# Kernel optimization log

Measured on AMD Instinct MI355X. Metric: run time of the kernel, lower is better.

The kernel has to match this reference:

```python
import jax, jax.numpy as jnp
import numpy as np
from jax.scipy.special import logsumexp

T = 8192        # trajectory length
S_DIM = 256     # state feature dim
B_OPT = 64      # number of options b
N_ACT = 64      # number of actions
STOP_IX = 0     # STOP_NET_STOP_IX
CONT_IX = 1     # STOP_NET_CONTINUE_IX


def setup_inputs() -> dict:
    key = jax.random.key(0)
    k1, k2, k3, k4, k5 = jax.random.split(key, 5)
    s_i = jax.random.normal(k1, (T + 1, S_DIM), dtype=jnp.float32)
    W_action = jax.random.normal(k2, (S_DIM, B_OPT, N_ACT), dtype=jnp.float32) * 0.02
    W_stop = jax.random.normal(k3, (S_DIM, B_OPT, 2), dtype=jnp.float32) * 0.02
    W_start = jax.random.normal(k4, (S_DIM, B_OPT), dtype=jnp.float32) * 0.02
    actions = jax.random.randint(k5, (T,), 0, N_ACT, dtype=jnp.int32)
    return {"s_i": s_i, "W_action": W_action, "W_stop": W_stop,
            "W_start": W_start, "actions": actions, "lengths": T}


def reference(s_i, W_action, W_stop, W_start, actions, lengths):
    # control_net heads: per-state, per-option log-probabilities
    action_logps = jax.nn.log_softmax(jnp.einsum('ts,sbn->tbn', s_i, W_action), axis=-1)  # (T+1, b, n_act)
    stop_logps = jax.nn.log_softmax(jnp.einsum('ts,sbc->tbc', s_i, W_stop), axis=-1)      # (T+1, b, 2)
    start_logps = jax.nn.log_softmax(jnp.einsum('ts,sb->tb', s_i, W_start), axis=-1)      # (T+1, b)

    Tn = actions.shape[0]
    # emission logp of the taken action at each step: (T, b)
    emit = jnp.take_along_axis(action_logps[:Tn], actions[:, None, None].astype(jnp.int32), axis=2)[:, :, 0]

    f0 = start_logps[0] + emit[0]  # (b,)
    eye = jnp.eye(B_OPT, dtype=bool)
    neg_inf = jnp.float32(-jnp.inf)

    def step(f_prev, xs):
        beta, one_minus_beta, start, em = xs
        # trans[i, j] = logaddexp(beta_i + start_j, delta_ij * log(1-beta_i))
        cont = jnp.where(eye, one_minus_beta[:, None], neg_inf)
        trans = jnp.logaddexp(beta[:, None] + start[None, :], cont)
        f = logsumexp(f_prev[:, None] + trans + em[None, :], axis=0)
        return f, None

    xs = (stop_logps[1:Tn, :, STOP_IX], stop_logps[1:Tn, :, CONT_IX],
          start_logps[1:Tn], emit[1:])
    f, _ = jax.lax.scan(step, f0, xs)

    total_logp = logsumexp(f + stop_logps[Tn, :, STOP_IX])
    return -total_logp
```

## Files before the change

### kernel.cpp

```cpp
#include <hip/hip_runtime.h>
#include <stdint.h>


typedef short bf16x8 __attribute__((ext_vector_type(8)));
typedef float f32x4  __attribute__((ext_vector_type(4)));
typedef unsigned short u16;

#define T_LEN 8192
#define SDIM  256

#define WS_SBF    0
#define WS_WAT    4227072
#define WS_WSMT   6324224
#define WS_PE     6422528
#define WS_PS     8519680
#define WS_PB     10617088
#define WS_PC     12714496
#define WS_MOUT   14811904
#define WS_LSC    16909056
#define WS_GOUT   WS_PC
#define WS_GLSC   (WS_PC + 262144)

__device__ inline u16 f2bf(float f) {
  union { float f; uint32_t u; } v; v.f = f;
  uint32_t u = v.u;
  return (u16)((u + 0x7fffu + ((u >> 16) & 1u)) >> 16);
}

__global__ void conv_s(const float* __restrict__ s_i, u16* __restrict__ s_bf) {
  int idx = blockIdx.x * 256 + threadIdx.x;
  int t = idx >> 8;
  float v = (t < T_LEN + 1) ? s_i[idx] : 0.f;
  s_bf[idx] = f2bf(v);
}

__global__ void conv_wa(const float* __restrict__ Wa, u16* __restrict__ wa_t) {
  int idx = blockIdx.x * 256 + threadIdx.x;
  int s = idx >> 12, bn = idx & 4095;
  wa_t[bn * 256 + s] = f2bf(Wa[idx]);
}

__global__ void conv_wsm(const float* __restrict__ Wstop, const float* __restrict__ Wstart,
                         u16* __restrict__ wsm_t) {
  int idx = blockIdx.x * 256 + threadIdx.x;
  int col = idx >> 8, s = idx & 255;
  float v;
  if (col < 64)       v = Wstart[s * 64 + col];
  else if (col < 128) v = Wstop[s * 128 + (col - 64) * 2 + 0];
  else                v = Wstop[s * 128 + (col - 128) * 2 + 1];
  wsm_t[col * 256 + s] = f2bf(v);
}

__global__ __launch_bounds__(256, 4) void act_gemm(
    const u16* __restrict__ s_bf, const u16* __restrict__ wa_t,
    const int* __restrict__ actions, float* __restrict__ peT) {
  __shared__ uint4 ldsB[64 * 32];
  const int tid = threadIdx.x;
  const int lane = tid & 63;
  const int wm = tid >> 6;
  const int g = lane >> 4, c = lane & 15;

  int bid = blockIdx.x;
  int swz = (bid & 7) * 512 + (bid >> 3);
  const int t0 = (swz >> 6) * 128;
  const int b0 = swz & 63;

  const int tbase = t0 + wm * 32;

  int act[2][4];
#pragma unroll
  for (int mf = 0; mf < 2; ++mf)
#pragma unroll
    for (int q = 0; q < 4; ++q)
      act[mf][q] = actions[tbase + mf * 16 + g * 4 + q];

  const u16* aRow0 = s_bf + (size_t)(tbase + c) * 256;
  const u16* aRow1 = s_bf + (size_t)(tbase + 16 + c) * 256;

  bf16x8 af0[2][4];
#pragma unroll
  for (int ks = 0; ks < 4; ++ks) {
    af0[0][ks] = *(const bf16x8*)(aRow0 + ks * 32 + g * 8);
    af0[1][ks] = *(const bf16x8*)(aRow1 + ks * 32 + g * 8);
  }

  {
    const u16* bsrc = wa_t + (size_t)b0 * 64 * 256;
#pragma unroll
    for (int it = 0; it < 8; ++it) {
      int i = tid + 256 * it;
      int r = i >> 5, s = i & 31;
      ldsB[r * 32 + (s ^ (r & 7))] = *(const uint4*)(bsrc + r * 256 + s * 8);
    }
  }
  __syncthreads();

  f32x4 acc[2][4];
#pragma unroll
  for (int mf = 0; mf < 2; ++mf)
#pragma unroll
    for (int nf = 0; nf < 4; ++nf) acc[mf][nf] = (f32x4){0.f, 0.f, 0.f, 0.f};

  bf16x8 af1[2][4];
#pragma unroll
  for (int ks = 0; ks < 4; ++ks) {
    af1[0][ks] = *(const bf16x8*)(aRow0 + 128 + ks * 32 + g * 8);
    af1[1][ks] = *(const bf16x8*)(aRow1 + 128 + ks * 32 + g * 8);
  }

#pragma unroll
  for (int ks = 0; ks < 4; ++ks) {
#pragma unroll
    for (int nf = 0; nf < 4; ++nf) {
      int rr = nf * 16 + c;
      bf16x8 bfv = *(const bf16x8*)&ldsB[rr * 32 + ((ks * 4 + g) ^ (rr & 7))];
      acc[0][nf] = __builtin_amdgcn_mfma_f32_16x16x32_bf16(af0[0][ks], bfv, acc[0][nf], 0, 0, 0);
      acc[1][nf] = __builtin_amdgcn_mfma_f32_16x16x32_bf16(af0[1][ks], bfv, acc[1][nf], 0, 0, 0);
    }
  }
#pragma unroll
  for (int ks = 0; ks < 4; ++ks) {
#pragma unroll
    for (int nf = 0; nf < 4; ++nf) {
      int rr = nf * 16 + c;
      bf16x8 bfv = *(const bf16x8*)&ldsB[rr * 32 + (((ks + 4) * 4 + g) ^ (rr & 7))];
      acc[0][nf] = __builtin_amdgcn_mfma_f32_16x16x32_bf16(af1[0][ks], bfv, acc[0][nf], 0, 0, 0);
      acc[1][nf] = __builtin_amdgcn_mfma_f32_16x16x32_bf16(af1[1][ks], bfv, acc[1][nf], 0, 0, 0);
    }
  }

  const size_t pebase = (size_t)b0 * 8192;
#pragma unroll
  for (int mf = 0; mf < 2; ++mf) {
#pragma unroll
    for (int q = 0; q < 4; ++q) {
      float e0 = __expf(acc[mf][0][q]);
      float e1 = __expf(acc[mf][1][q]);
      float e2 = __expf(acc[mf][2][q]);
      float e3 = __expf(acc[mf][3][q]);
      float s = (e0 + e1) + (e2 + e3);
#pragma unroll
      for (int d = 1; d < 16; d <<= 1) s += __shfl_xor(s, d);
      int a = act[mf][q];
      int acf = a >> 4;
      float esel = (acf == 0) ? e0 : (acf == 1) ? e1 : (acf == 2) ? e2 : e3;
      if (c == (a & 15))
        peT[pebase + tbase + mf * 16 + g * 4 + q] = esel / s;
    }
  }
}

__global__ __launch_bounds__(256) void small_gemm(
    const u16* __restrict__ s_bf, const u16* __restrict__ wsm_t,
    float* __restrict__ ps, float* __restrict__ pb, float* __restrict__ pc) {
  __shared__ uint4 ldsA[64 * 16];
  __shared__ uint4 ldsB[192 * 16];
  const int t0 = blockIdx.x * 64;
  const int tid = threadIdx.x;
  const int lane = tid & 63, w = tid >> 6;
  const int g = lane >> 4, c = lane & 15;

  f32x4 acc[12];
#pragma unroll
  for (int i = 0; i < 12; ++i) acc[i] = (f32x4){0.f, 0.f, 0.f, 0.f};

  for (int kh = 0; kh < 2; ++kh) {
    if (kh) __syncthreads();
    for (int i = tid; i < 64 * 16; i += 256) {
      int row = i >> 4, u = i & 15;
      ldsA[(row * 16 + u) ^ (row & 7)] =
          *(const uint4*)(s_bf + (size_t)(t0 + row) * 256 + kh * 128 + u * 8);
    }
    for (int i = tid; i < 192 * 16; i += 256) {
      int row = i >> 4, u = i & 15;
      ldsB[(row * 16 + u) ^ (row & 7)] =
          *(const uint4*)(wsm_t + (size_t)row * 256 + kh * 128 + u * 8);
    }
    __syncthreads();
#pragma unroll
    for (int kk = 0; kk < 4; ++kk) {
      int u = kk * 4 + g;
      int arow = w * 16 + c;
      bf16x8 af = *(const bf16x8*)&ldsA[(arow * 16 + u) ^ (arow & 7)];
#pragma unroll
      for (int cf = 0; cf < 12; ++cf) {
        int brow = cf * 16 + c;
        bf16x8 bfr = *(const bf16x8*)&ldsB[(brow * 16 + u) ^ (brow & 7)];
        acc[cf] = __builtin_amdgcn_mfma_f32_16x16x32_bf16(af, bfr, acc[cf], 0, 0, 0);
      }
    }
  }

#pragma unroll
  for (int q = 0; q < 4; ++q) {
    int t = t0 + w * 16 + g * 4 + q;
    float v0 = acc[0][q], v1 = acc[1][q], v2 = acc[2][q], v3 = acc[3][q];
    float m = fmaxf(fmaxf(v0, v1), fmaxf(v2, v3));
#pragma unroll
    for (int d = 1; d < 16; d <<= 1) m = fmaxf(m, __shfl_xor(m, d));
    float s = __expf(v0 - m) + __expf(v1 - m) + __expf(v2 - m) + __expf(v3 - m);
#pragma unroll
    for (int d = 1; d < 16; d <<= 1) s += __shfl_xor(s, d);
    float lse = m + __logf(s);
    if (t <= T_LEN) {
      ps[t * 64 + 0 * 16 + c] = __expf(v0 - lse);
      ps[t * 64 + 1 * 16 + c] = __expf(v1 - lse);
      ps[t * 64 + 2 * 16 + c] = __expf(v2 - lse);
      ps[t * 64 + 3 * 16 + c] = __expf(v3 - lse);
#pragma unroll
      for (int bf = 0; bf < 4; ++bf) {
        float l0 = acc[4 + bf][q], l1 = acc[8 + bf][q];
        float d01 = l0 - l1;
        pb[t * 64 + bf * 16 + c] = 1.f / (1.f + __expf(-d01));
        pc[t * 64 + bf * 16 + c] = 1.f / (1.f + __expf(d01));
      }
    }
  }
}

__global__ __launch_bounds__(256) void chunk_kernel(
    const float* __restrict__ peT, const float* __restrict__ ps,
    const float* __restrict__ pb, const float* __restrict__ pc,
    float* __restrict__ Mout, float* __restrict__ lscale) {
  __shared__ float scal[64 * 196];
  __shared__ float part[2][256];
  __shared__ float mxs[4];
  const int ck = blockIdx.x;
  const int tid = threadIdx.x;
  const int lane = tid & 63;
  const int w = tid >> 6;
  const int tlo = ck * 64 + 1;

#pragma unroll
  for (int it = 0; it < 16; ++it) {
    int i = tid + 256 * it;
    int st = i >> 6, j = i & 63;
    int t = tlo + st;
    if (t <= T_LEN - 1) {
      int base = t * 64 + j;
      scal[st * 196 + j]       = pb[base];
      scal[st * 196 + 64 + j]  = pc[base];
      scal[st * 196 + 128 + j] = ps[base];
    } else {
      scal[st * 196 + j]       = 0.f;
      scal[st * 196 + 64 + j]  = 1.f;
      scal[st * 196 + 128 + j] = 0.f;
    }
  }
  __syncthreads();
#pragma unroll
  for (int it = 0; it < 16; ++it) {
    int i = tid + 256 * it;
    int j = i >> 6, st = i & 63;
    int t = tlo + st;
    if (t <= T_LEN - 1) {
      float e = peT[(size_t)j * 8192 + t];
      scal[st * 196 + 64 + j]  *= e;
      scal[st * 196 + 128 + j] *= e;
    }
  }
  __syncthreads();

  float M[16];
#pragma unroll
  for (int jj = 0; jj < 16; ++jj) M[jj] = ((w * 16 + jj) == lane) ? 1.f : 0.f;
  float lsc = 0.f;
  int pbuf = 0;

  for (int st = 0; st < 64; ++st) {
    const float* sb = &scal[st * 196];
    float p0 = 0.f, p1 = 0.f, p2 = 0.f, p3 = 0.f;
#pragma unroll
    for (int q = 0; q < 4; ++q) {
      float4 bq = *(const float4*)(sb + w * 16 + q * 4);
      p0 = fmaf(bq.x, M[q * 4 + 0], p0);
      p1 = fmaf(bq.y, M[q * 4 + 1], p1);
      p2 = fmaf(bq.z, M[q * 4 + 2], p2);
      p3 = fmaf(bq.w, M[q * 4 + 3], p3);
    }
    part[pbuf][w * 64 + lane] = (p0 + p1) + (p2 + p3);
    __syncthreads();
    float wv = part[pbuf][lane] + part[pbuf][64 + lane] +
               part[pbuf][128 + lane] + part[pbuf][192 + lane];
    pbuf ^= 1;
#pragma unroll
    for (int q = 0; q < 4; ++q) {
      float4 ecq = *(const float4*)(sb + 64 + w * 16 + q * 4);
      float4 esq = *(const float4*)(sb + 128 + w * 16 + q * 4);
      M[q * 4 + 0] = fmaf(ecq.x, M[q * 4 + 0], esq.x * wv);
      M[q * 4 + 1] = fmaf(ecq.y, M[q * 4 + 1], esq.y * wv);
      M[q * 4 + 2] = fmaf(ecq.z, M[q * 4 + 2], esq.z * wv);
      M[q * 4 + 3] = fmaf(ecq.w, M[q * 4 + 3], esq.w * wv);
    }
    if ((st & 7) == 7) {
      float mx = M[0];
#pragma unroll
      for (int jj = 1; jj < 16; ++jj) mx = fmaxf(mx, M[jj]);
#pragma unroll
      for (int d = 1; d < 64; d <<= 1) mx = fmaxf(mx, __shfl_xor(mx, d));
      if (lane == 0) mxs[w] = mx;
      __syncthreads();
      float bm = fmaxf(fmaxf(mxs[0], mxs[1]), fmaxf(mxs[2], mxs[3]));
      float inv = 1.f / bm;
#pragma unroll
      for (int jj = 0; jj < 16; ++jj) M[jj] *= inv;
      lsc += __logf(bm);
    }
  }

  float* out = Mout + (size_t)ck * 4096;
#pragma unroll
  for (int q = 0; q < 4; ++q) {
    float4 v = make_float4(M[q * 4 + 0], M[q * 4 + 1], M[q * 4 + 2], M[q * 4 + 3]);
    *(float4*)(out + lane * 64 + w * 16 + q * 4) = v;
  }
  if (tid == 0) lscale[ck] = lsc;
}

__global__ __launch_bounds__(256) void group_combine(
    const float* __restrict__ Mout, const float* __restrict__ lscale,
    float* __restrict__ Gout, float* __restrict__ glsc) {
  const int g = blockIdx.x;
  const int tid = threadIdx.x;
  const int j = tid & 63;
  const int w = tid >> 6;
  __shared__ float Xa[64 * 68];
  __shared__ float Xb[64 * 68];
  __shared__ float Ma[64 * 68];
  __shared__ float Mb[64 * 68];
  __shared__ float red[4];

  {
    const float* M0 = Mout + (size_t)(8 * g) * 4096;
    const float* M1 = Mout + (size_t)(8 * g + 1) * 4096;
    for (int idx = tid; idx < 4096; idx += 256) {
      int i = idx >> 6, r = idx & 63;
      Xa[r * 68 + i] = M0[idx];
      Ma[i * 68 + r] = M1[idx];
    }
  }
  __syncthreads();

  float lsc = 0.f;
  float* Xcur = Xa; float* Xnxt = Xb;
  float* Mcur = Ma; float* Mnxt = Mb;

  for (int m = 1; m < 8; ++m) {
    float4 pf[4];
    if (m < 7) {
      const float* Mn = Mout + (size_t)(8 * g + m + 1) * 4096;
#pragma unroll
      for (int ii = 0; ii < 4; ++ii)
        pf[ii] = *(const float4*)(Mn + tid * 4 + 1024 * ii);
    }

    float acc[16];
#pragma unroll
    for (int i = 0; i < 16; ++i) acc[i] = 0.f;

#pragma unroll 4
    for (int k = 0; k < 64; ++k) {
      float mv = Mcur[k * 68 + j];
      const float* xr = Xcur + k * 68 + (w << 4);
      float4 x0 = *(const float4*)(xr + 0);
      float4 x1 = *(const float4*)(xr + 4);
      float4 x2 = *(const float4*)(xr + 8);
      float4 x3 = *(const float4*)(xr + 12);
      acc[0]  = fmaf(mv, x0.x, acc[0]);  acc[1]  = fmaf(mv, x0.y, acc[1]);
      acc[2]  = fmaf(mv, x0.z, acc[2]);  acc[3]  = fmaf(mv, x0.w, acc[3]);
      acc[4]  = fmaf(mv, x1.x, acc[4]);  acc[5]  = fmaf(mv, x1.y, acc[5]);
      acc[6]  = fmaf(mv, x1.z, acc[6]);  acc[7]  = fmaf(mv, x1.w, acc[7]);
      acc[8]  = fmaf(mv, x2.x, acc[8]);  acc[9]  = fmaf(mv, x2.y, acc[9]);
      acc[10] = fmaf(mv, x2.z, acc[10]); acc[11] = fmaf(mv, x2.w, acc[11]);
      acc[12] = fmaf(mv, x3.x, acc[12]); acc[13] = fmaf(mv, x3.y, acc[13]);
      acc[14] = fmaf(mv, x3.z, acc[14]); acc[15] = fmaf(mv, x3.w, acc[15]);
    }

    float lm = acc[0];
#pragma unroll
    for (int i = 1; i < 16; ++i) lm = fmaxf(lm, acc[i]);
#pragma unroll
    for (int d = 1; d < 64; d <<= 1) lm = fmaxf(lm, __shfl_xor(lm, d));
    if ((tid & 63) == 0) red[w] = lm;
    __syncthreads();
    float bm = fmaxf(fmaxf(red[0], red[1]), fmaxf(red[2], red[3]));
    float inv = 1.f / bm;
    lsc += __logf(bm);
#pragma unroll
    for (int i = 0; i < 16; ++i)
      Xnxt[j * 68 + (w << 4) + i] = acc[i] * inv;
    if (m < 7) {
#pragma unroll
      for (int ii = 0; ii < 4; ++ii) {
        int idx = tid * 4 + 1024 * ii;
        int k = idx >> 6, jj = idx & 63;
        *(float4*)(Mnxt + k * 68 + jj) = pf[ii];
      }
    }
    __syncthreads();
    float* t = Xcur; Xcur = Xnxt; Xnxt = t;
    float* tm = Mcur; Mcur = Mnxt; Mnxt = tm;
  }

  float* out = Gout + (size_t)g * 4096;
  for (int idx = tid; idx < 4096; idx += 256) {
    int i = idx >> 6, r = idx & 63;
    out[idx] = Xcur[r * 68 + i];
  }
  if (tid == 0) {
    float s = lsc;
#pragma unroll
    for (int m = 0; m < 8; ++m) s += lscale[8 * g + m];
    glsc[g] = s;
  }
}

__global__ __launch_bounds__(256) void final_combine(
    const float* __restrict__ Gout, const float* __restrict__ glsc,
    const float* __restrict__ peT, const float* __restrict__ ps,
    const float* __restrict__ pb, float* __restrict__ out) {
  const int tid = threadIdx.x;
  const int j = tid & 63, w = tid >> 6;
  __shared__ float vsh[64];
  __shared__ float part[4 * 64];
  if (tid < 64) vsh[tid] = ps[tid] * peT[(size_t)tid * 8192];
  __syncthreads();
  double lsc = 0.0;
  for (int gph = 0; gph < 16; ++gph) {
    const float* Gc = Gout + (size_t)gph * 4096;
    const int k0 = w << 4;
    float a0 = 0.f, a1 = 0.f, a2 = 0.f, a3 = 0.f;
#pragma unroll
    for (int kk = 0; kk < 16; kk += 4) {
      a0 = fmaf(vsh[k0 + kk + 0], Gc[(k0 + kk + 0) * 64 + j], a0);
      a1 = fmaf(vsh[k0 + kk + 1], Gc[(k0 + kk + 1) * 64 + j], a1);
      a2 = fmaf(vsh[k0 + kk + 2], Gc[(k0 + kk + 2) * 64 + j], a2);
      a3 = fmaf(vsh[k0 + kk + 3], Gc[(k0 + kk + 3) * 64 + j], a3);
    }
    part[w * 64 + j] = (a0 + a1) + (a2 + a3);
    __syncthreads();
    if (w == 0) {
      float u = part[j] + part[64 + j] + part[128 + j] + part[192 + j];
      float mx = u;
#pragma unroll
      for (int d = 1; d < 64; d <<= 1) mx = fmaxf(mx, __shfl_xor(mx, d));
      vsh[j] = u / mx;
      lsc += (double)__logf(mx) + (double)glsc[gph];
    }
    __syncthreads();
  }
  if (w == 0) {
    float z = vsh[j] * pb[T_LEN * 64 + j];
#pragma unroll
    for (int d = 1; d < 64; d <<= 1) z += __shfl_xor(z, d);
    if (j == 0) out[0] = (float)(-((double)logf(z) + lsc));
  }
}

extern "C" void kernel_launch(void* const* d_in, const int* in_sizes, int n_in,
                              void* d_out, int out_size, void* d_ws, size_t ws_size,
                              hipStream_t stream) {
  const float* s_i      = (const float*)d_in[0];
  const float* W_action = (const float*)d_in[1];
  const float* W_stop   = (const float*)d_in[2];
  const float* W_start  = (const float*)d_in[3];
  const int*   actions  = (const int*)d_in[4];

  char* ws = (char*)d_ws;
  u16*   s_bf  = (u16*)(ws + WS_SBF);
  u16*   wa_t  = (u16*)(ws + WS_WAT);
  u16*   wsm_t = (u16*)(ws + WS_WSMT);
  float* peT   = (float*)(ws + WS_PE);
  float* ps    = (float*)(ws + WS_PS);
  float* pb    = (float*)(ws + WS_PB);
  float* pc    = (float*)(ws + WS_PC);
  float* Mout  = (float*)(ws + WS_MOUT);
  float* lsc   = (float*)(ws + WS_LSC);
  float* Gout  = (float*)(ws + WS_GOUT);
  float* glsc  = (float*)(ws + WS_GLSC);

  conv_s<<<8256, 256, 0, stream>>>(s_i, s_bf);
  conv_wa<<<4096, 256, 0, stream>>>(W_action, wa_t);
  conv_wsm<<<192, 256, 0, stream>>>(W_stop, W_start, wsm_t);
  small_gemm<<<129, 256, 0, stream>>>(s_bf, wsm_t, ps, pb, pc);
  act_gemm<<<4096, 256, 0, stream>>>(s_bf, wa_t, actions, peT);
  chunk_kernel<<<128, 256, 0, stream>>>(peT, ps, pb, pc, Mout, lsc);
  group_combine<<<16, 256, 0, stream>>>(Mout, lsc, Gout, glsc);
  final_combine<<<1, 256, 0, stream>>>(Gout, glsc, peT, ps, pb, (float*)d_out);
}
```

Measured before the change: 152.9 us.

## Make action GEMM persistent with option weights held in registers

Restructures act_gemm from 4096 short-lived blocks that stage a 64x256 weight tile through LDS into 512 blocks of 512 threads. Each block keeps one option's weight tile in registers and loops over 8 time tiles of 128 steps. This drops the LDS staging, the barrier and the repeated weight loads per block, and it amortises launch cost. In exchange, register pressure rises sharply (bq alone is 32 bf16x8 vectors per lane), which may limit occupancy or cause spills. Parallelism also falls to 512 blocks, each running a serial loop over time tiles.

```diff
diff --git a/kernel.cpp b/kernel.cpp
--- a/kernel.cpp
+++ b/kernel.cpp
@@ -51,101 +51,69 @@
   wsm_t[col * 256 + s] = f2bf(v);
 }
 
-__global__ __launch_bounds__(256, 4) void act_gemm(
+__global__ __launch_bounds__(512, 2) void act_gemm(
     const u16* __restrict__ s_bf, const u16* __restrict__ wa_t,
     const int* __restrict__ actions, float* __restrict__ peT) {
-  __shared__ uint4 ldsB[64 * 32];
   const int tid = threadIdx.x;
   const int lane = tid & 63;
-  const int wm = tid >> 6;
+  const int wmv = tid >> 6;
   const int g = lane >> 4, c = lane & 15;
 
-  int bid = blockIdx.x;
-  int swz = (bid & 7) * 512 + (bid >> 3);
-  const int t0 = (swz >> 6) * 128;
-  const int b0 = swz & 63;
-
-  const int tbase = t0 + wm * 32;
-
-  int act[2][4];
-#pragma unroll
-  for (int mf = 0; mf < 2; ++mf)
-#pragma unroll
-    for (int q = 0; q < 4; ++q)
-      act[mf][q] = actions[tbase + mf * 16 + g * 4 + q];
-
-  const u16* aRow0 = s_bf + (size_t)(tbase + c) * 256;
-  const u16* aRow1 = s_bf + (size_t)(tbase + 16 + c) * 256;
-
-  bf16x8 af0[2][4];
-#pragma unroll
-  for (int ks = 0; ks < 4; ++ks) {
-    af0[0][ks] = *(const bf16x8*)(aRow0 + ks * 32 + g * 8);
-    af0[1][ks] = *(const bf16x8*)(aRow1 + ks * 32 + g * 8);
-  }
-
+  const int bid = blockIdx.x;
+  const int slab = bid & 7;
+  const int b0 = bid >> 3;
+
+  bf16x8 bq[8][4];
   {
-    const u16* bsrc = wa_t + (size_t)b0 * 64 * 256;
-#pragma unroll
-    for (int it = 0; it < 8; ++it) {
-      int i = tid + 256 * it;
-      int r = i >> 5, s = i & 31;
-      ldsB[r * 32 + (s ^ (r & 7))] = *(const uint4*)(bsrc + r * 256 + s * 8);
-    }
-  }
-  __syncthreads();
-
-  f32x4 acc[2][4];
-#pragma unroll
-  for (int mf = 0; mf < 2; ++mf)
-#pragma unroll
-    for (int nf = 0; nf < 4; ++nf) acc[mf][nf] = (f32x4){0.f, 0.f, 0.f, 0.f};
-
-  bf16x8 af1[2][4];
-#pragma unroll
-  for (int ks = 0; ks < 4; ++ks) {
-    af1[0][ks] = *(const bf16x8*)(aRow0 + 128 + ks * 32 + g * 8);
-    af1[1][ks] = *(const bf16x8*)(aRow1 + 128 + ks * 32 + g * 8);
-  }
-
-#pragma unroll
-  for (int ks = 0; ks < 4; ++ks) {
-#pragma unroll
-    for (int nf = 0; nf < 4; ++nf) {
-      int rr = nf * 16 + c;
-      bf16x8 bfv = *(const bf16x8*)&ldsB[rr * 32 + ((ks * 4 + g) ^ (rr & 7))];
-      acc[0][nf] = __builtin_amdgcn_mfma_f32_16x16x32_bf16(af0[0][ks], bfv, acc[0][nf], 0, 0, 0);
-      acc[1][nf] = __builtin_amdgcn_mfma_f32_16x16x32_bf16(af0[1][ks], bfv, acc[1][nf], 0, 0, 0);
-    }
-  }
-#pragma unroll
-  for (int ks = 0; ks < 4; ++ks) {
-#pragma unroll
-    for (int nf = 0; nf < 4; ++nf) {
-      int rr = nf * 16 + c;
-      bf16x8 bfv = *(const bf16x8*)&ldsB[rr * 32 + (((ks + 4) * 4 + g) ^ (rr & 7))];
-      acc[0][nf] = __builtin_amdgcn_mfma_f32_16x16x32_bf16(af1[0][ks], bfv, acc[0][nf], 0, 0, 0);
-      acc[1][nf] = __builtin_amdgcn_mfma_f32_16x16x32_bf16(af1[1][ks], bfv, acc[1][nf], 0, 0, 0);
-    }
+    const u16* bbase = wa_t + (size_t)b0 * 64 * 256 + (size_t)c * 256 + g * 8;
+#pragma unroll
+    for (int ks = 0; ks < 8; ++ks)
+#pragma unroll
+      for (int nf = 0; nf < 4; ++nf)
+        bq[ks][nf] = *(const bf16x8*)(bbase + nf * 16 * 256 + ks * 32);
   }
 
   const size_t pebase = (size_t)b0 * 8192;
-#pragma unroll
-  for (int mf = 0; mf < 2; ++mf) {
+
+  for (int it = 0; it < 8; ++it) {
+    const int tbase = slab * 1024 + it * 128 + wmv * 16;
+
+    const u16* arow = s_bf + (size_t)(tbase + c) * 256 + g * 8;
+    bf16x8 af[8];
+#pragma unroll
+    for (int ks = 0; ks < 8; ++ks)
+      af[ks] = *(const bf16x8*)(arow + ks * 32);
+
+    int a0 = actions[tbase + g * 4 + 0];
+    int a1 = actions[tbase + g * 4 + 1];
+    int a2 = actions[tbase + g * 4 + 2];
+    int a3 = actions[tbase + g * 4 + 3];
+
+    f32x4 acc[4];
+#pragma unroll
+    for (int nf = 0; nf < 4; ++nf) acc[nf] = (f32x4){0.f, 0.f, 0.f, 0.f};
+
+#pragma unroll
+    for (int ks = 0; ks < 8; ++ks)
+#pragma unroll
+      for (int nf = 0; nf < 4; ++nf)
+        acc[nf] = __builtin_amdgcn_mfma_f32_16x16x32_bf16(af[ks], bq[ks][nf], acc[nf], 0, 0, 0);
+
+    const int acts[4] = {a0, a1, a2, a3};
 #pragma unroll
     for (int q = 0; q < 4; ++q) {
-      float e0 = __expf(acc[mf][0][q]);
-      float e1 = __expf(acc[mf][1][q]);
-      float e2 = __expf(acc[mf][2][q]);
-      float e3 = __expf(acc[mf][3][q]);
+      float e0 = __expf(acc[0][q]);
+      float e1 = __expf(acc[1][q]);
+      float e2 = __expf(acc[2][q]);
+      float e3 = __expf(acc[3][q]);
       float s = (e0 + e1) + (e2 + e3);
 #pragma unroll
       for (int d = 1; d < 16; d <<= 1) s += __shfl_xor(s, d);
-      int a = act[mf][q];
+      int a = acts[q];
       int acf = a >> 4;
       float esel = (acf == 0) ? e0 : (acf == 1) ? e1 : (acf == 2) ? e2 : e3;
       if (c == (a & 15))
-        peT[pebase + tbase + mf * 16 + g * 4 + q] = esel / s;
+        peT[pebase + tbase + g * 4 + q] = esel / s;
     }
   }
 }
@@ -483,7 +451,7 @@
   conv_wa<<<4096, 256, 0, stream>>>(W_action, wa_t);
   conv_wsm<<<192, 256, 0, stream>>>(W_stop, W_start, wsm_t);
   small_gemm<<<129, 256, 0, stream>>>(s_bf, wsm_t, ps, pb, pc);
-  act_gemm<<<4096, 256, 0, stream>>>(s_bf, wa_t, actions, peT);
+  act_gemm<<<512, 512, 0, stream>>>(s_bf, wa_t, actions, peT);
   chunk_kernel<<<128, 256, 0, stream>>>(peT, ps, pb, pc, Mout, lsc);
   group_combine<<<16, 256, 0, stream>>>(Mout, lsc, Gout, glsc);
   final_combine<<<1, 256, 0, stream>>>(Gout, glsc, peT, ps, pb, (float*)d_out);
```

After: 174.7 us. 1.14x slower.

## Make act_gemm persistent over time slabs with double-buffered A fragments

Applied to the files above, without the earlier changes.

The action GEMM now launches 512 blocks instead of 4096. Each block loads one option's 64x256 weight tile into LDS once and loops over 8 time tiles of 128 rows, so the LDS weight tile is reused 8 times. While computing the current tile it prefetches the next tile's A fragments into registers, and launch bounds drop to 2 blocks per SM to make room for the doubled register set. The aim is fewer redundant weight loads and less per-block setup. The cost is lower occupancy, and 512 blocks may not fill a 256-CU device well.

```diff
diff --git a/kernel.cpp b/kernel.cpp
--- a/kernel.cpp
+++ b/kernel.cpp
@@ -51,38 +51,18 @@
   wsm_t[col * 256 + s] = f2bf(v);
 }
 
-__global__ __launch_bounds__(256, 4) void act_gemm(
+__global__ __launch_bounds__(256, 2) void act_gemm(
     const u16* __restrict__ s_bf, const u16* __restrict__ wa_t,
     const int* __restrict__ actions, float* __restrict__ peT) {
   __shared__ uint4 ldsB[64 * 32];
   const int tid = threadIdx.x;
   const int lane = tid & 63;
-  const int wm = tid >> 6;
+  const int wmv = tid >> 6;
   const int g = lane >> 4, c = lane & 15;
 
-  int bid = blockIdx.x;
-  int swz = (bid & 7) * 512 + (bid >> 3);
-  const int t0 = (swz >> 6) * 128;
-  const int b0 = swz & 63;
-
-  const int tbase = t0 + wm * 32;
-
-  int act[2][4];
-#pragma unroll
-  for (int mf = 0; mf < 2; ++mf)
-#pragma unroll
-    for (int q = 0; q < 4; ++q)
-      act[mf][q] = actions[tbase + mf * 16 + g * 4 + q];
-
-  const u16* aRow0 = s_bf + (size_t)(tbase + c) * 256;
-  const u16* aRow1 = s_bf + (size_t)(tbase + 16 + c) * 256;
-
-  bf16x8 af0[2][4];
-#pragma unroll
-  for (int ks = 0; ks < 4; ++ks) {
-    af0[0][ks] = *(const bf16x8*)(aRow0 + ks * 32 + g * 8);
-    af0[1][ks] = *(const bf16x8*)(aRow1 + ks * 32 + g * 8);
-  }
+  const int bid = blockIdx.x;
+  const int slab = bid & 7;
+  const int b0 = bid >> 3;
 
   {
     const u16* bsrc = wa_t + (size_t)b0 * 64 * 256;
@@ -93,59 +73,76 @@
       ldsB[r * 32 + (s ^ (r & 7))] = *(const uint4*)(bsrc + r * 256 + s * 8);
     }
   }
+
+  const size_t pebase = (size_t)b0 * 8192;
+  const int tw = slab * 1024 + wmv * 32;
+
+  bf16x8 af[2][8], afn[2][8];
+  {
+    const u16* ar0 = s_bf + (size_t)(tw + c) * 256 + g * 8;
+    const u16* ar1 = s_bf + (size_t)(tw + 16 + c) * 256 + g * 8;
+#pragma unroll
+    for (int ks = 0; ks < 8; ++ks) {
+      af[0][ks] = *(const bf16x8*)(ar0 + ks * 32);
+      af[1][ks] = *(const bf16x8*)(ar1 + ks * 32);
+    }
+  }
   __syncthreads();
 
-  f32x4 acc[2][4];
-#pragma unroll
-  for (int mf = 0; mf < 2; ++mf)
-#pragma unroll
-    for (int nf = 0; nf < 4; ++nf) acc[mf][nf] = (f32x4){0.f, 0.f, 0.f, 0.f};
-
-  bf16x8 af1[2][4];
-#pragma unroll
-  for (int ks = 0; ks < 4; ++ks) {
-    af1[0][ks] = *(const bf16x8*)(aRow0 + 128 + ks * 32 + g * 8);
-    af1[1][ks] = *(const bf16x8*)(aRow1 + 128 + ks * 32 + g * 8);
-  }
-
-#pragma unroll
-  for (int ks = 0; ks < 4; ++ks) {
-#pragma unroll
-    for (int nf = 0; nf < 4; ++nf) {
-      int rr = nf * 16 + c;
-      bf16x8 bfv = *(const bf16x8*)&ldsB[rr * 32 + ((ks * 4 + g) ^ (rr & 7))];
-      acc[0][nf] = __builtin_amdgcn_mfma_f32_16x16x32_bf16(af0[0][ks], bfv, acc[0][nf], 0, 0, 0);
-      acc[1][nf] = __builtin_amdgcn_mfma_f32_16x16x32_bf16(af0[1][ks], bfv, acc[1][nf], 0, 0, 0);
-    }
-  }
-#pragma unroll
-  for (int ks = 0; ks < 4; ++ks) {
-#pragma unroll
-    for (int nf = 0; nf < 4; ++nf) {
-      int rr = nf * 16 + c;
-      bf16x8 bfv = *(const bf16x8*)&ldsB[rr * 32 + (((ks + 4) * 4 + g) ^ (rr & 7))];
-      acc[0][nf] = __builtin_amdgcn_mfma_f32_16x16x32_bf16(af1[0][ks], bfv, acc[0][nf], 0, 0, 0);
-      acc[1][nf] = __builtin_amdgcn_mfma_f32_16x16x32_bf16(af1[1][ks], bfv, acc[1][nf], 0, 0, 0);
-    }
-  }
-
-  const size_t pebase = (size_t)b0 * 8192;
-#pragma unroll
-  for (int mf = 0; mf < 2; ++mf) {
-#pragma unroll
-    for (int q = 0; q < 4; ++q) {
-      float e0 = __expf(acc[mf][0][q]);
-      float e1 = __expf(acc[mf][1][q]);
-      float e2 = __expf(acc[mf][2][q]);
-      float e3 = __expf(acc[mf][3][q]);
-      float s = (e0 + e1) + (e2 + e3);
-#pragma unroll
-      for (int d = 1; d < 16; d <<= 1) s += __shfl_xor(s, d);
-      int a = act[mf][q];
-      int acf = a >> 4;
-      float esel = (acf == 0) ? e0 : (acf == 1) ? e1 : (acf == 2) ? e2 : e3;
-      if (c == (a & 15))
-        peT[pebase + tbase + mf * 16 + g * 4 + q] = esel / s;
+#pragma unroll 1
+  for (int it = 0; it < 8; ++it) {
+    const int tbase = tw + it * 128;
+
+    if (it < 7) {
+      const u16* ar0 = s_bf + (size_t)(tbase + 128 + c) * 256 + g * 8;
+      const u16* ar1 = s_bf + (size_t)(tbase + 144 + c) * 256 + g * 8;
+#pragma unroll
+      for (int ks = 0; ks < 8; ++ks) {
+        afn[0][ks] = *(const bf16x8*)(ar0 + ks * 32);
+        afn[1][ks] = *(const bf16x8*)(ar1 + ks * 32);
+      }
+    }
+
+    f32x4 acc[2][4];
+#pragma unroll
+    for (int mf = 0; mf < 2; ++mf)
+#pragma unroll
+      for (int nf = 0; nf < 4; ++nf) acc[mf][nf] = (f32x4){0.f, 0.f, 0.f, 0.f};
+
+#pragma unroll
+    for (int ks = 0; ks < 8; ++ks) {
+#pragma unroll
+      for (int nf = 0; nf < 4; ++nf) {
+        int rr = nf * 16 + c;
+        bf16x8 bfv = *(const bf16x8*)&ldsB[rr * 32 + ((ks * 4 + g) ^ (rr & 7))];
+        acc[0][nf] = __builtin_amdgcn_mfma_f32_16x16x32_bf16(af[0][ks], bfv, acc[0][nf], 0, 0, 0);
+        acc[1][nf] = __builtin_amdgcn_mfma_f32_16x16x32_bf16(af[1][ks], bfv, acc[1][nf], 0, 0, 0);
+      }
+    }
+
+#pragma unroll
+    for (int mf = 0; mf < 2; ++mf) {
+#pragma unroll
+      for (int q = 0; q < 4; ++q) {
+        float e0 = __expf(acc[mf][0][q]);
+        float e1 = __expf(acc[mf][1][q]);
+        float e2 = __expf(acc[mf][2][q]);
+        float e3 = __expf(acc[mf][3][q]);
+        float s = (e0 + e1) + (e2 + e3);
+#pragma unroll
+        for (int d = 1; d < 16; d <<= 1) s += __shfl_xor(s, d);
+        int a = actions[tbase + mf * 16 + g * 4 + q];
+        int acf = a >> 4;
+        float esel = (acf == 0) ? e0 : (acf == 1) ? e1 : (acf == 2) ? e2 : e3;
+        if (c == (a & 15))
+          peT[pebase + tbase + mf * 16 + g * 4 + q] = esel / s;
+      }
+    }
+
+#pragma unroll
+    for (int ks = 0; ks < 8; ++ks) {
+      af[0][ks] = afn[0][ks];
+      af[1][ks] = afn[1][ks];
     }
   }
 }
@@ -483,7 +480,7 @@
   conv_wa<<<4096, 256, 0, stream>>>(W_action, wa_t);
   conv_wsm<<<192, 256, 0, stream>>>(W_stop, W_start, wsm_t);
   small_gemm<<<129, 256, 0, stream>>>(s_bf, wsm_t, ps, pb, pc);
-  act_gemm<<<4096, 256, 0, stream>>>(s_bf, wa_t, actions, peT);
+  act_gemm<<<512, 256, 0, stream>>>(s_bf, wa_t, actions, peT);
   chunk_kernel<<<128, 256, 0, stream>>>(peT, ps, pb, pc, Mout, lsc);
   group_combine<<<16, 256, 0, stream>>>(Mout, lsc, Gout, glsc);
   final_combine<<<1, 256, 0, stream>>>(Gout, glsc, peT, ps, pb, (float*)d_out);
```

Result: slower. 179.2 us (+17.2%).
